# Optimization experiments

Measured on AMD Instinct MI355X. Metric: run time of the kernel, lower is better.

## Reference

```python
import jax, jax.numpy as jnp
import numpy as np

N = 50000   # total nodes
G = 100     # graphs
E = 64      # embedding size
L = 4       # message-passing layers
MU = 100000 # unary atoms
ME = 200000 # binary atoms (edges)


def setup_inputs() -> dict:
    key = jax.random.key(0)
    ks = jax.random.split(key, 16)

    def w(k, shape):
        fan_in = shape[0]
        return (jax.random.normal(k, shape, jnp.float32) / np.sqrt(fan_in)).astype(jnp.float32)

    inp = {
        "rel_unary": jax.random.randint(ks[0], (MU, 1), 0, N, dtype=jnp.int32),
        "rel_edge": jax.random.randint(ks[1], (ME, 2), 0, N, dtype=jnp.int32),
        "graph_ids": jnp.repeat(jnp.arange(G, dtype=jnp.int32), N // G),
        "num_graphs": G,
        # unary relation message MLP (E -> E -> E)
        "Wm1_u": w(ks[2], (E, E)), "bm1_u": jnp.zeros((E,), jnp.float32),
        "Wm2_u": w(ks[3], (E, E)), "bm2_u": jnp.zeros((E,), jnp.float32),
        # binary relation message MLP (2E -> 2E -> 2E), one message per argument position
        "Wm1_e": w(ks[4], (2 * E, 2 * E)), "bm1_e": jnp.zeros((2 * E,), jnp.float32),
        "Wm2_e": w(ks[5], (2 * E, 2 * E)), "bm2_e": jnp.zeros((2 * E,), jnp.float32),
        # node update MLP (2E -> E -> E)
        "Wu1": w(ks[6], (2 * E, E)), "bu1": jnp.zeros((E,), jnp.float32),
        "Wu2": w(ks[7], (E, E)), "bu2": jnp.zeros((E,), jnp.float32),
        # LayerNorm
        "ln_w": jnp.ones((E,), jnp.float32), "ln_b": jnp.zeros((E,), jnp.float32),
        # SumReadout projection (E -> E)
        "Wr": w(ks[8], (E, E)), "br": jnp.zeros((E,), jnp.float32),
        # global update MLP (2E -> E -> E)
        "Wg1": w(ks[9], (2 * E, E)), "bg1": jnp.zeros((E,), jnp.float32),
        "Wg2": w(ks[10], (E, E)), "bg2": jnp.zeros((E,), jnp.float32),
    }
    return inp


def _mlp(x, W1, b1, W2, b2):
    return jax.nn.relu(x @ W1 + b1) @ W2 + b2


def _ln(x, w, b):
    mu = x.mean(-1, keepdims=True)
    v = ((x - mu) ** 2).mean(-1, keepdims=True)
    return (x - mu) * jax.lax.rsqrt(v + 1e-5) * w + b


def reference(rel_unary, rel_edge, graph_ids, num_graphs,
              Wm1_u, bm1_u, Wm2_u, bm2_u,
              Wm1_e, bm1_e, Wm2_e, bm2_e,
              Wu1, bu1, Wu2, bu2,
              ln_w, ln_b, Wr, br,
              Wg1, bg1, Wg2, bg2):
    n = graph_ids.shape[0]
    e = ln_w.shape[0]
    me = rel_edge.shape[0]
    h = jnp.zeros((n, e), jnp.float32)  # initial node embeddings (as in torch code)
    for _ in range(L):
        # --- message: per-relation MLP over concatenated argument embeddings ---
        msg_u = _mlp(h[rel_unary[:, 0]], Wm1_u, bm1_u, Wm2_u, bm2_u)          # [MU, E]
        xe = h[rel_edge].reshape(me, 2 * e)                                    # [ME, 2E]
        msg_e = _mlp(xe, Wm1_e, bm1_e, Wm2_e, bm2_e).reshape(me * 2, e)        # one msg per arg
        # --- aggregation: scatter-sum messages to destination nodes ---
        all_msgs = jnp.concatenate([msg_u, msg_e], axis=0)
        all_idx = jnp.concatenate([rel_unary[:, 0], rel_edge.reshape(-1)], axis=0)
        agg = jax.ops.segment_sum(all_msgs, all_idx, num_segments=n)           # [N, E]
        # --- update MLP + LayerNorm ---
        nxt = _ln(_mlp(jnp.concatenate([h, agg], axis=1), Wu1, bu1, Wu2, bu2), ln_w, ln_b)
        # --- global readout + broadcast update ---
        g = jax.ops.segment_sum(h, graph_ids, num_segments=num_graphs) @ Wr + br  # [G, E]
        gin = jnp.concatenate([h, g[graph_ids]], axis=1)                       # repeat_interleave as gather
        gm = _ln(_mlp(gin, Wg1, bg1, Wg2, bg2), ln_w, ln_b)
        # residual update
        h = h + nxt + gm
    return h
```

## Files before the change

### kernel.cpp

```cpp
#include <hip/hip_runtime.h>


#define E 64
#define TWO_E 128

__device__ __forceinline__ void sfma32(float (&acc)[32], float xu, const float* w) {
  #pragma unroll
  for (int i = 0; i < 32; ++i) acc[i] = fmaf(xu, w[i], acc[i]);
}
__device__ __forceinline__ void sfma16(float (&acc)[16], float xu, const float* w) {
  #pragma unroll
  for (int i = 0; i < 16; ++i) acc[i] = fmaf(xu, w[i], acc[i]);
}

__global__ void k_zero(float4* __restrict__ p, int n4) {
  int i = blockIdx.x * blockDim.x + threadIdx.x;
  if (i < n4) p[i] = make_float4(0.f, 0.f, 0.f, 0.f);
}

__global__ void k_count_e(const int* __restrict__ rel_e, int* __restrict__ cpos0,
                          int* __restrict__ cpos1, int me) {
  int e = blockIdx.x * blockDim.x + threadIdx.x;
  if (e >= me) return;
  int2 sd = ((const int2*)rel_e)[e];
  atomicAdd(&cpos0[sd.x], 1);
  atomicAdd(&cpos1[sd.y], 1);
}
__global__ void k_count_u(const int* __restrict__ rel_u, int* __restrict__ cnt_u, int mu) {
  int m = blockIdx.x * blockDim.x + threadIdx.x;
  if (m >= mu) return;
  atomicAdd(&cnt_u[rel_u[m]], 1);
}

__global__ void __launch_bounds__(256) k_bsum(
    const int* __restrict__ cpos0, const int* __restrict__ cpos1,
    int* __restrict__ bsum, int nn, int nb) {
  __shared__ int l0[256], l1[256];
  int t = threadIdx.x, b = blockIdx.x;
  int i = b * 256 + t;
  l0[t] = (i < nn) ? cpos0[i] : 0;
  l1[t] = (i < nn) ? cpos1[i] : 0;
  __syncthreads();
  for (int off = 128; off > 0; off >>= 1) {
    if (t < off) { l0[t] += l0[t + off]; l1[t] += l1[t + off]; }
    __syncthreads();
  }
  if (t == 0) { bsum[b] = l0[0]; bsum[nb + b] = l1[0]; }
}

__global__ void __launch_bounds__(256) k_scanblk(
    const int* __restrict__ bsum, int* __restrict__ boff, int nb) {
  __shared__ int l0[256], l1[256];
  int t = threadIdx.x;
  int o0 = (t < nb) ? bsum[t] : 0;
  int o1 = (t < nb) ? bsum[nb + t] : 0;
  l0[t] = o0; l1[t] = o1;
  __syncthreads();
  for (int off = 1; off < 256; off <<= 1) {
    int v0 = (t >= off) ? l0[t - off] : 0;
    int v1 = (t >= off) ? l1[t - off] : 0;
    __syncthreads();
    l0[t] += v0; l1[t] += v1;
    __syncthreads();
  }
  if (t < nb) { boff[t] = l0[t] - o0; boff[nb + t] = l1[t] - o1; }
}

__global__ void __launch_bounds__(256) k_wstart(
    const int* __restrict__ cpos0, const int* __restrict__ cpos1,
    const int* __restrict__ boff,
    int* __restrict__ startp, int* __restrict__ startp0, int* __restrict__ startp1,
    int* __restrict__ cur0, int* __restrict__ cur1, int nn, int nb, int me) {
  __shared__ int l0[256], l1[256];
  int t = threadIdx.x, b = blockIdx.x;
  int i = b * 256 + t;
  int c0 = (i < nn) ? cpos0[i] : 0;
  int c1 = (i < nn) ? cpos1[i] : 0;
  l0[t] = c0; l1[t] = c1;
  __syncthreads();
  for (int off = 1; off < 256; off <<= 1) {
    int v0 = (t >= off) ? l0[t - off] : 0;
    int v1 = (t >= off) ? l1[t - off] : 0;
    __syncthreads();
    l0[t] += v0; l1[t] += v1;
    __syncthreads();
  }
  if (i < nn) {
    int s0 = boff[b] + l0[t] - c0;
    int s1 = boff[nb + b] + l1[t] - c1;
    startp0[i] = s0; startp1[i] = s1; startp[i] = s0 + s1;
    cur0[i] = s0; cur1[i] = s1;
  }
  if (i == nn) { startp0[nn] = me; startp1[nn] = me; startp[nn] = 2 * me; }
}

__global__ void k_fill_e(const int* __restrict__ rel_e,
                         const int* __restrict__ startp, const int* __restrict__ startp0,
                         const int* __restrict__ startp1, const int* __restrict__ cpos0,
                         int* __restrict__ cur0, int* __restrict__ cur1,
                         int* __restrict__ ord0, int* __restrict__ pos0,
                         int* __restrict__ posE1, int me) {
  int e = blockIdx.x * blockDim.x + threadIdx.x;
  if (e >= me) return;
  int2 sd = ((const int2*)rel_e)[e];
  int s = sd.x, d = sd.y;
  int i0 = atomicAdd(&cur0[s], 1);
  ord0[i0] = e;
  pos0[i0] = startp[s] + (i0 - startp0[s]);
  int i1 = atomicAdd(&cur1[d], 1);
  posE1[e] = startp[d] + cpos0[d] + (i1 - startp1[d]);
}

__global__ void k_mlp0(const float* __restrict__ b1u, const float* __restrict__ W2u,
                       const float* __restrict__ b2u,
                       const float* __restrict__ b1e, const float* __restrict__ W2e,
                       const float* __restrict__ b2e,
                       const float* __restrict__ br,
                       float* __restrict__ mu0, float* __restrict__ me0,
                       float* __restrict__ g, int gn) {
  __shared__ float hu[64], he[128];
  int t = threadIdx.x;
  if (t < 64) hu[t] = fmaxf(b1u[t], 0.f);
  he[t] = fmaxf(b1e[t], 0.f);
  __syncthreads();
  if (t < 64) {
    float a = b2u[t];
    for (int k = 0; k < 64; ++k) a = fmaf(hu[k], W2u[k * 64 + t], a);
    mu0[t] = a;
  }
  float a = b2e[t];
  for (int k = 0; k < 128; ++k) a = fmaf(he[k], W2e[k * TWO_E + t], a);
  me0[t] = a;
  if (t < 64) {
    float b = br[t];
    for (int gi = 0; gi < gn; ++gi) g[gi * 64 + t] = b;
  }
}

__global__ void k_agg0(const int* __restrict__ cnt_u, const int* __restrict__ cpos0,
                       const int* __restrict__ cpos1, const float* __restrict__ mu0,
                       const float* __restrict__ me0, float* __restrict__ agg, int nn) {
  int i = blockIdx.x * blockDim.x + threadIdx.x;
  int n = i >> 4, j4 = i & 15;
  if (n >= nn) return;
  float cu = (float)cnt_u[n], c0 = (float)cpos0[n], c1 = (float)cpos1[n];
  float4 m = ((const float4*)mu0)[j4];
  float4 a = ((const float4*)me0)[j4];
  float4 b = ((const float4*)(me0 + 64))[j4];
  ((float4*)agg)[i] = make_float4(cu * m.x + c0 * a.x + c1 * b.x,
                                  cu * m.y + c0 * a.y + c1 * b.y,
                                  cu * m.z + c0 * a.z + c1 * b.z,
                                  cu * m.w + c0 * a.w + c1 * b.w);
}

__global__ void __launch_bounds__(512) k_edge_pab(
    const int* __restrict__ rel_e, const int* __restrict__ ord0,
    const int* __restrict__ pos0, const int* __restrict__ posE1,
    const float* __restrict__ Pab,
    const float* __restrict__ W2, const float* __restrict__ b2,
    float* __restrict__ msgbuf, int me)
{
  __shared__ __align__(16) float tl[64 * 132];
  const int tid = threadIdx.x;
  const int lane = tid & 63;
  const int wq = __builtin_amdgcn_readfirstlane(tid >> 6);
  const int i = blockIdx.x * 64 + lane;
  const bool valid = (i < me);
  const int ic = valid ? i : (me - 1);
  const int e = ord0[ic];
  const int2 sd = ((const int2*)rel_e)[e];
  const int s = sd.x, d = sd.y;
  const int p_s = pos0[ic];
  const int p_d = posE1[e];

  {
    const float4* pa = (const float4*)(Pab + (size_t)s * 256 + wq * 16);
    const float4* pb = (const float4*)(Pab + (size_t)d * 256 + 128 + wq * 16);
    float4* trow = (float4*)&tl[lane * 132 + wq * 16];
    #pragma unroll
    for (int u = 0; u < 4; ++u) {
      float4 va = pa[u], vb = pb[u];
      trow[u] = make_float4(fmaxf(va.x + vb.x, 0.f), fmaxf(va.y + vb.y, 0.f),
                            fmaxf(va.z + vb.z, 0.f), fmaxf(va.w + vb.w, 0.f));
    }
  }
  __syncthreads();

  float o[16];
  {
    const float* bp = b2 + wq * 16;
    #pragma unroll
    for (int u = 0; u < 16; ++u) o[u] = bp[u];
  }
  {
    const float4* tr = (const float4*)&tl[lane * 132];
    const float* w = W2 + wq * 16;
    #pragma unroll 4
    for (int kk = 0; kk < 32; ++kk) {
      float4 tv = tr[kk];
      sfma16(o, tv.x, w);
      sfma16(o, tv.y, w + TWO_E);
      sfma16(o, tv.z, w + 2 * TWO_E);
      sfma16(o, tv.w, w + 3 * TWO_E);
      w += 4 * TWO_E;
    }
  }
  if (valid) {
    int p0 = (wq >= 4) ? p_d : p_s;
    float4* mp = (float4*)(msgbuf + (size_t)p0 * E + (wq & 3) * 16);
    #pragma unroll
    for (int u = 0; u < 4; ++u)
      mp[u] = make_float4(o[4*u], o[4*u+1], o[4*u+2], o[4*u+3]);
  }
}

__global__ void __launch_bounds__(256) k_edge_fb(
    const int* __restrict__ rel_e, const int* __restrict__ ord0,
    const int* __restrict__ pos0, const int* __restrict__ posE1,
    const float* __restrict__ h,
    const float* __restrict__ W1, const float* __restrict__ b1,
    const float* __restrict__ W2, const float* __restrict__ b2,
    float* __restrict__ msgbuf, int me)
{
  __shared__ __align__(16) float tl[64 * 132];
  const int tid = threadIdx.x;
  const int lane = tid & 63;
  const int wq = __builtin_amdgcn_readfirstlane(tid >> 6);
  const int i = blockIdx.x * 64 + lane;
  const bool valid = (i < me);
  const int ic = valid ? i : (me - 1);
  const int e = ord0[ic];
  const int2 sd = ((const int2*)rel_e)[e];
  const int s = sd.x, d = sd.y;
  const int p_s = pos0[ic];
  const int p_d = posE1[e];
  const float4* xs4 = (const float4*)(h + (size_t)s * E);
  const float4* xd4 = (const float4*)(h + (size_t)d * E);

  float acc[32];
  {
    const float* bp = b1 + wq * 32;
    #pragma unroll
    for (int u = 0; u < 32; ++u) acc[u] = bp[u];
  }
  {
    const float* w = W1 + wq * 32;
    #pragma unroll 2
    for (int k4 = 0; k4 < 16; ++k4) {
      float4 xv = xs4[k4];
      sfma32(acc, xv.x, w);
      sfma32(acc, xv.y, w + TWO_E);
      sfma32(acc, xv.z, w + 2 * TWO_E);
      sfma32(acc, xv.w, w + 3 * TWO_E);
      w += 4 * TWO_E;
    }
    #pragma unroll 2
    for (int k4 = 0; k4 < 16; ++k4) {
      float4 xv = xd4[k4];
      sfma32(acc, xv.x, w);
      sfma32(acc, xv.y, w + TWO_E);
      sfma32(acc, xv.z, w + 2 * TWO_E);
      sfma32(acc, xv.w, w + 3 * TWO_E);
      w += 4 * TWO_E;
    }
  }
  {
    float4* trow = (float4*)&tl[lane * 132 + wq * 32];
    #pragma unroll
    for (int u = 0; u < 8; ++u)
      trow[u] = make_float4(fmaxf(acc[4*u], 0.f), fmaxf(acc[4*u+1], 0.f),
                            fmaxf(acc[4*u+2], 0.f), fmaxf(acc[4*u+3], 0.f));
  }
  __syncthreads();

  float o[32];
  {
    const float* bp = b2 + wq * 32;
    #pragma unroll
    for (int u = 0; u < 32; ++u) o[u] = bp[u];
  }
  {
    const float4* tr = (const float4*)&tl[lane * 132];
    const float* w = W2 + wq * 32;
    #pragma unroll 4
    for (int kk = 0; kk < 32; ++kk) {
      float4 tv = tr[kk];
      sfma32(o, tv.x, w);
      sfma32(o, tv.y, w + TWO_E);
      sfma32(o, tv.z, w + 2 * TWO_E);
      sfma32(o, tv.w, w + 3 * TWO_E);
      w += 4 * TWO_E;
    }
  }
  if (valid) {
    int p0 = (wq >> 1) ? p_d : p_s;
    float4* mp = (float4*)(msgbuf + (size_t)p0 * E + (wq & 1) * 32);
    #pragma unroll
    for (int u = 0; u < 8; ++u)
      mp[u] = make_float4(o[4*u], o[4*u+1], o[4*u+2], o[4*u+3]);
  }
}

__global__ void __launch_bounds__(256) k_gather(
    const float* __restrict__ msgbuf, const int* __restrict__ startp,
    float* __restrict__ agg, int nn)
{
  int wave = threadIdx.x >> 6;
  int j = threadIdx.x & 63;
  int n = blockIdx.x * 4 + wave;
  if (n >= nn) return;
  int s0 = startp[n], s1 = startp[n + 1];
  int cnt = s1 - s0;
  const float* p = msgbuf + (size_t)s0 * E + j;
  float v0 = 0.f, v1 = 0.f;
  int i = 0;
  for (; i + 1 < cnt; i += 2) { v0 += p[0]; v1 += p[E]; p += 2 * E; }
  if (i < cnt) v0 += p[0];
  agg[(size_t)n * E + j] += v0 + v1;
}

__global__ void __launch_bounds__(256) k_readout_g(
    const float* __restrict__ h, const int* __restrict__ gids,
    const float* __restrict__ Wr, const float* __restrict__ br,
    float* __restrict__ g, int nn, int npg)
{
  __shared__ float ls[4][64];
  __shared__ float grow[64];
  const int j = threadIdx.x & 63;
  const int w = threadIdx.x >> 6;
  const int base = blockIdx.x * npg;
  float acc = 0.f;
  for (int i = w; i < npg; i += 4) {
    int node = base + i;
    if (node < nn) acc += h[(size_t)node * 64 + j];
  }
  ls[w][j] = acc;
  __syncthreads();
  if (w == 0) grow[j] = ls[0][j] + ls[1][j] + ls[2][j] + ls[3][j];
  __syncthreads();
  float p = 0.f;
  #pragma unroll
  for (int kk = 0; kk < 16; ++kk) {
    int k = w * 16 + kk;
    p = fmaf(grow[k], Wr[k * 64 + j], p);
  }
  ls[w][j] = p;
  __syncthreads();
  if (w == 0) {
    int gout = gids[base];
    g[gout * 64 + j] = ls[0][j] + ls[1][j] + ls[2][j] + ls[3][j] + br[j];
  }
}

template <bool DO_NEXT>
__global__ void __launch_bounds__(256) k_update(
    float* __restrict__ h, float* __restrict__ agg,
    const float* __restrict__ gvec, const int* __restrict__ gids,
    const float* __restrict__ Wu1, const float* __restrict__ bu1,
    const float* __restrict__ Wu2, const float* __restrict__ bu2,
    const float* __restrict__ Wg1, const float* __restrict__ bg1,
    const float* __restrict__ Wg2, const float* __restrict__ bg2,
    const float* __restrict__ lnw, const float* __restrict__ lnb,
    const int* __restrict__ cnt_u,
    const float* __restrict__ Wmu1, const float* __restrict__ bmu1,
    const float* __restrict__ Wmu2, const float* __restrict__ bmu2,
    const float* __restrict__ W1e, const float* __restrict__ b1e,
    float* __restrict__ Pab, int do_pab, int nn)
{
  __shared__ __align__(16) float tl[64 * 68];
  __shared__ float st[64 * 9];
  const int tid = threadIdx.x;
  const int lane = tid & 63;
  const int q = __builtin_amdgcn_readfirstlane(tid >> 6);
  const int n = blockIdx.x * 64 + lane;
  const bool valid = (n < nn);
  const int ncl = valid ? n : (nn - 1);
  const int gid = gids[ncl];
  const float4* hx = (const float4*)(h + (size_t)ncl * E);
  const float4* ax = (const float4*)(agg + (size_t)ncl * E);
  const float4* gx = (const float4*)(gvec + (size_t)gid * E);

  float res[16];

  #pragma unroll
  for (int pass = 0; pass < 2; ++pass) {
    const float* W1 = (pass == 0) ? Wu1 : Wg1;
    const float* B1 = (pass == 0) ? bu1 : bg1;
    const float* W2 = (pass == 0) ? Wu2 : Wg2;
    const float* B2 = (pass == 0) ? bu2 : bg2;
    const float4* xb = (pass == 0) ? ax : gx;

    float acc[16];
    {
      const float* bp = B1 + q * 16;
      #pragma unroll
      for (int u = 0; u < 16; ++u) acc[u] = bp[u];
    }
    {
      const float* w = W1 + q * 16;
      #pragma unroll 2
      for (int k4 = 0; k4 < 16; ++k4) {
        float4 xv = hx[k4];
        sfma16(acc, xv.x, w);
        sfma16(acc, xv.y, w + E);
        sfma16(acc, xv.z, w + 2 * E);
        sfma16(acc, xv.w, w + 3 * E);
        w += 4 * E;
      }
      #pragma unroll 2
      for (int k4 = 0; k4 < 16; ++k4) {
        float4 xv = xb[k4];
        sfma16(acc, xv.x, w);
        sfma16(acc, xv.y, w + E);
        sfma16(acc, xv.z, w + 2 * E);
        sfma16(acc, xv.w, w + 3 * E);
        w += 4 * E;
      }
    }
    {
      float4* trow = (float4*)&tl[lane * 68 + q * 16];
      #pragma unroll
      for (int u = 0; u < 4; ++u)
        trow[u] = make_float4(fmaxf(acc[4*u], 0.f), fmaxf(acc[4*u+1], 0.f),
                              fmaxf(acc[4*u+2], 0.f), fmaxf(acc[4*u+3], 0.f));
    }
    __syncthreads();

    float o[16];
    {
      const float* bp = B2 + q * 16;
      #pragma unroll
      for (int u = 0; u < 16; ++u) o[u] = bp[u];
    }
    {
      const float4* tr = (const float4*)&tl[lane * 68];
      const float* w = W2 + q * 16;
      #pragma unroll 4
      for (int kk = 0; kk < 16; ++kk) {
        float4 tv = tr[kk];
        sfma16(o, tv.x, w);
        sfma16(o, tv.y, w + E);
        sfma16(o, tv.z, w + 2 * E);
        sfma16(o, tv.w, w + 3 * E);
        w += 4 * E;
      }
    }

    float s1 = 0.f;
    #pragma unroll
    for (int u = 0; u < 16; ++u) s1 += o[u];
    st[lane * 9 + q] = s1;
    __syncthreads();
    float mu = (st[lane * 9 + 0] + st[lane * 9 + 1] +
                st[lane * 9 + 2] + st[lane * 9 + 3]) * (1.f / E);
    float s2 = 0.f;
    #pragma unroll
    for (int u = 0; u < 16; ++u) { float dm = o[u] - mu; s2 += dm * dm; }
    st[lane * 9 + 4 + q] = s2;
    __syncthreads();
    float var = (st[lane * 9 + 4] + st[lane * 9 + 5] +
                 st[lane * 9 + 6] + st[lane * 9 + 7]) * (1.f / E);
    float rs = rsqrtf(var + 1e-5f);
    {
      const float* lw = lnw + q * 16;
      const float* lb = lnb + q * 16;
      #pragma unroll
      for (int u = 0; u < 16; ++u) {
        float v = (o[u] - mu) * rs * lw[u] + lb[u];
        if (pass == 0) res[u] = v; else res[u] += v;
      }
    }
  }

  float hnew[16];
  {
    const float4* hr = (const float4*)(h + (size_t)ncl * E + q * 16);
    #pragma unroll
    for (int u = 0; u < 4; ++u) {
      float4 hv = hr[u];
      hnew[4*u+0] = hv.x + res[4*u+0];
      hnew[4*u+1] = hv.y + res[4*u+1];
      hnew[4*u+2] = hv.z + res[4*u+2];
      hnew[4*u+3] = hv.w + res[4*u+3];
    }
  }
  if (valid) {
    float4* hw = (float4*)(h + (size_t)n * E + q * 16);
    #pragma unroll
    for (int u = 0; u < 4; ++u)
      hw[u] = make_float4(hnew[4*u], hnew[4*u+1], hnew[4*u+2], hnew[4*u+3]);
  }

  if (DO_NEXT) {
    {
      float4* trow = (float4*)&tl[lane * 68 + q * 16];
      #pragma unroll
      for (int u = 0; u < 4; ++u)
        trow[u] = make_float4(hnew[4*u], hnew[4*u+1], hnew[4*u+2], hnew[4*u+3]);
    }
    __syncthreads();

    float acc[16];
    {
      const float* bp = bmu1 + q * 16;
      #pragma unroll
      for (int u = 0; u < 16; ++u) acc[u] = bp[u];
    }
    {
      const float4* tr = (const float4*)&tl[lane * 68];
      const float* w = Wmu1 + q * 16;
      #pragma unroll 4
      for (int kk = 0; kk < 16; ++kk) {
        float4 tv = tr[kk];
        sfma16(acc, tv.x, w);
        sfma16(acc, tv.y, w + E);
        sfma16(acc, tv.z, w + 2 * E);
        sfma16(acc, tv.w, w + 3 * E);
        w += 4 * E;
      }
    }

    if (do_pab) {
      #pragma unroll 1
      for (int c = 0; c < 2; ++c) {
        const int col = q * 64 + c * 32;
        const int rbase = (col < 128) ? 0 : 64;
        const int cw = (col < 128) ? col : (col - 128);
        float pacc[32];
        if (col < 128) {
          const float* bp = b1e + cw;
          #pragma unroll
          for (int u = 0; u < 32; ++u) pacc[u] = bp[u];
        } else {
          #pragma unroll
          for (int u = 0; u < 32; ++u) pacc[u] = 0.f;
        }
        const float4* tr = (const float4*)&tl[lane * 68];
        const float* w = W1e + rbase * TWO_E + cw;
        #pragma unroll 4
        for (int kk = 0; kk < 16; ++kk) {
          float4 tv = tr[kk];
          sfma32(pacc, tv.x, w);
          sfma32(pacc, tv.y, w + TWO_E);
          sfma32(pacc, tv.z, w + 2 * TWO_E);
          sfma32(pacc, tv.w, w + 3 * TWO_E);
          w += 4 * TWO_E;
        }
        if (valid) {
          float4* op = (float4*)(Pab + (size_t)n * 256 + col);
          #pragma unroll
          for (int u = 0; u < 8; ++u)
            op[u] = make_float4(pacc[4*u], pacc[4*u+1], pacc[4*u+2], pacc[4*u+3]);
        }
      }
    }
    __syncthreads();
    {
      float4* trow = (float4*)&tl[lane * 68 + q * 16];
      #pragma unroll
      for (int u = 0; u < 4; ++u)
        trow[u] = make_float4(fmaxf(acc[4*u], 0.f), fmaxf(acc[4*u+1], 0.f),
                              fmaxf(acc[4*u+2], 0.f), fmaxf(acc[4*u+3], 0.f));
    }
    __syncthreads();

    float o[16];
    {
      const float* bp = bmu2 + q * 16;
      #pragma unroll
      for (int u = 0; u < 16; ++u) o[u] = bp[u];
    }
    {
      const float4* tr = (const float4*)&tl[lane * 68];
      const float* w = Wmu2 + q * 16;
      #pragma unroll 4
      for (int kk = 0; kk < 16; ++kk) {
        float4 tv = tr[kk];
        sfma16(o, tv.x, w);
        sfma16(o, tv.y, w + E);
        sfma16(o, tv.z, w + 2 * E);
        sfma16(o, tv.w, w + 3 * E);
        w += 4 * E;
      }
    }
    if (valid) {
      float cf = (float)cnt_u[n];
      float4* ap = (float4*)(agg + (size_t)n * E + q * 16);
      #pragma unroll
      for (int u = 0; u < 4; ++u)
        ap[u] = make_float4(o[4*u] * cf, o[4*u+1] * cf, o[4*u+2] * cf, o[4*u+3] * cf);
    }
  }
}

extern "C" void kernel_launch(void* const* d_in, const int* in_sizes, int n_in,
                              void* d_out, int out_size, void* d_ws, size_t ws_size,
                              hipStream_t stream) {
  (void)n_in; (void)out_size;
  const int*   rel_u = (const int*)d_in[0];
  const int*   rel_e = (const int*)d_in[1];
  const int*   gids  = (const int*)d_in[2];
  const float* Wm1_u = (const float*)d_in[4];
  const float* bm1_u = (const float*)d_in[5];
  const float* Wm2_u = (const float*)d_in[6];
  const float* bm2_u = (const float*)d_in[7];
  const float* Wm1_e = (const float*)d_in[8];
  const float* bm1_e = (const float*)d_in[9];
  const float* Wm2_e = (const float*)d_in[10];
  const float* bm2_e = (const float*)d_in[11];
  const float* Wu1   = (const float*)d_in[12];
  const float* bu1   = (const float*)d_in[13];
  const float* Wu2   = (const float*)d_in[14];
  const float* bu2   = (const float*)d_in[15];
  const float* lnw   = (const float*)d_in[16];
  const float* lnb   = (const float*)d_in[17];
  const float* Wr    = (const float*)d_in[18];
  const float* br    = (const float*)d_in[19];
  const float* Wg1   = (const float*)d_in[20];
  const float* bg1   = (const float*)d_in[21];
  const float* Wg2   = (const float*)d_in[22];
  const float* bg2   = (const float*)d_in[23];

  const int MU_ = in_sizes[0];
  const int ME_ = in_sizes[1] / 2;
  const int NN  = in_sizes[2];
  const int GN  = 100;
  const int NPG = NN / GN;
  const int M2  = 2 * ME_;
  const int NB  = (NN + 255) / 256;
  const int NBW = (NN + 256) / 256;
  const int NBU = (NN + 63) / 64;

  float* h       = (float*)d_out;
  float* agg     = (float*)d_ws;
  float* g       = agg + (size_t)NN * E;
  float* mu0     = g + (size_t)GN * E;
  float* me0     = mu0 + 64;
  float* msgbuf  = me0 + TWO_E;
  int*   cpos0   = (int*)(msgbuf + (size_t)M2 * E);
  int*   cpos1   = cpos0 + NN;
  int*   cnt_u   = cpos1 + NN;
  int*   startp  = cnt_u + NN;
  int*   startp0 = startp + NN + 1;
  int*   startp1 = startp0 + NN + 1;
  int*   cur0    = startp1 + NN + 1;
  int*   cur1    = cur0 + NN + 1;
  int*   ord0    = cur1 + NN + 1;
  int*   pos0    = ord0 + ME_;
  int*   posE1   = pos0 + ME_;
  int*   bsum    = posE1 + ME_;
  int*   boff    = bsum + 2 * NB;
  size_t int_end = (size_t)(boff + 2 * NB - (int*)d_ws);
  size_t pab_off = (int_end + 3) & ~(size_t)3;
  float* Pab     = (float*)d_ws + pab_off;
  size_t need_pab = (pab_off + (size_t)NN * 256) * 4;
  const bool pab_mode = (ws_size >= need_pab);

  {
    int n4 = NN * E / 4;
    k_zero<<<(n4 + 255) / 256, 256, 0, stream>>>((float4*)h, n4);
  }
  {
    int n4 = (3 * NN + 4) / 4;
    k_zero<<<(n4 + 255) / 256, 256, 0, stream>>>((float4*)cpos0, n4);
  }
  k_count_e<<<(ME_ + 255) / 256, 256, 0, stream>>>(rel_e, cpos0, cpos1, ME_);
  k_count_u<<<(MU_ + 255) / 256, 256, 0, stream>>>(rel_u, cnt_u, MU_);
  k_bsum<<<NB, 256, 0, stream>>>(cpos0, cpos1, bsum, NN, NB);
  k_scanblk<<<1, 256, 0, stream>>>(bsum, boff, NB);
  k_wstart<<<NBW, 256, 0, stream>>>(cpos0, cpos1, boff, startp, startp0, startp1,
                                    cur0, cur1, NN, NB, ME_);
  k_fill_e<<<(ME_ + 255) / 256, 256, 0, stream>>>(
      rel_e, startp, startp0, startp1, cpos0, cur0, cur1, ord0, pos0, posE1, ME_);
  k_mlp0<<<1, 128, 0, stream>>>(bm1_u, Wm2_u, bm2_u, bm1_e, Wm2_e, bm2_e,
                                br, mu0, me0, g, GN);

  k_agg0<<<(NN * 16 + 255) / 256, 256, 0, stream>>>(cnt_u, cpos0, cpos1, mu0, me0, agg, NN);
  k_update<true><<<NBU, 256, 0, stream>>>(
      h, agg, g, gids, Wu1, bu1, Wu2, bu2, Wg1, bg1, Wg2, bg2, lnw, lnb,
      cnt_u, Wm1_u, bm1_u, Wm2_u, bm2_u, Wm1_e, bm1_e, Pab, pab_mode ? 1 : 0, NN);

  for (int l = 1; l < 4; ++l) {
    if (pab_mode)
      k_edge_pab<<<(ME_ + 63) / 64, 512, 0, stream>>>(
          rel_e, ord0, pos0, posE1, Pab, Wm2_e, bm2_e, msgbuf, ME_);
    else
      k_edge_fb<<<(ME_ + 63) / 64, 256, 0, stream>>>(
          rel_e, ord0, pos0, posE1, h, Wm1_e, bm1_e, Wm2_e, bm2_e, msgbuf, ME_);
    k_gather<<<(NN + 3) / 4, 256, 0, stream>>>(msgbuf, startp, agg, NN);
    k_readout_g<<<GN, 256, 0, stream>>>(h, gids, Wr, br, g, NN, NPG);
    if (l < 3)
      k_update<true><<<NBU, 256, 0, stream>>>(
          h, agg, g, gids, Wu1, bu1, Wu2, bu2, Wg1, bg1, Wg2, bg2, lnw, lnb,
          cnt_u, Wm1_u, bm1_u, Wm2_u, bm2_u, Wm1_e, bm1_e, Pab, pab_mode ? 1 : 0, NN);
    else
      k_update<false><<<NBU, 256, 0, stream>>>(
          h, agg, g, gids, Wu1, bu1, Wu2, bu2, Wg1, bg1, Wg2, bg2, lnw, lnb,
          cnt_u, Wm1_u, bm1_u, Wm2_u, bm2_u, Wm1_e, bm1_e, Pab, 0, NN);
  }
}
```

Before: 838.1 us.

## Run update and global MLPs concurrently on separate wave pairs in k_update

Previously all four waves ran the update MLP and then the global MLP in two sequential passes, each wave owning 16 output columns. Now waves 0-1 compute the update MLP and waves 2-3 the global MLP at the same time, each wave owning 32 columns, with a second LDS tile holding the global result for the residual sum. This halves the barrier-separated phases for the two MLPs but doubles per-thread accumulator registers and LDS use, which may lower occupancy.

```diff
diff --git a/kernel.cpp b/kernel.cpp
--- a/kernel.cpp
+++ b/kernel.cpp
@@ -367,163 +367,166 @@
     const float* __restrict__ W1e, const float* __restrict__ b1e,
     float* __restrict__ Pab, int do_pab, int nn)
 {
-  __shared__ __align__(16) float tl[64 * 68];
+  __shared__ __align__(16) float tlu[64 * 68];
+  __shared__ __align__(16) float tlg[64 * 68];
   __shared__ float st[64 * 9];
   const int tid = threadIdx.x;
   const int lane = tid & 63;
-  const int q = __builtin_amdgcn_readfirstlane(tid >> 6);
+  const int w = __builtin_amdgcn_readfirstlane(tid >> 6);
+  const int hf = w & 1;
+  const int pbase = w & 2;
+  const bool isU = (w < 2);
   const int n = blockIdx.x * 64 + lane;
   const bool valid = (n < nn);
   const int ncl = valid ? n : (nn - 1);
   const int gid = gids[ncl];
   const float4* hx = (const float4*)(h + (size_t)ncl * E);
-  const float4* ax = (const float4*)(agg + (size_t)ncl * E);
-  const float4* gx = (const float4*)(gvec + (size_t)gid * E);
-
-  float res[16];
-
-  #pragma unroll
-  for (int pass = 0; pass < 2; ++pass) {
-    const float* W1 = (pass == 0) ? Wu1 : Wg1;
-    const float* B1 = (pass == 0) ? bu1 : bg1;
-    const float* W2 = (pass == 0) ? Wu2 : Wg2;
-    const float* B2 = (pass == 0) ? bu2 : bg2;
-    const float4* xb = (pass == 0) ? ax : gx;
-
-    float acc[16];
+  const float4* xb = isU ? (const float4*)(agg + (size_t)ncl * E)
+                         : (const float4*)(gvec + (size_t)gid * E);
+  const float* W1 = isU ? Wu1 : Wg1;
+  const float* B1 = isU ? bu1 : bg1;
+  const float* W2 = isU ? Wu2 : Wg2;
+  const float* B2 = isU ? bu2 : bg2;
+  float* tlmine = isU ? tlu : tlg;
+
+  float acc[32];
+  {
+    const float* bp = B1 + hf * 32;
+    #pragma unroll
+    for (int u = 0; u < 32; ++u) acc[u] = bp[u];
+  }
+  {
+    const float* wp = W1 + hf * 32;
+    #pragma unroll 2
+    for (int k4 = 0; k4 < 16; ++k4) {
+      float4 xv = hx[k4];
+      sfma32(acc, xv.x, wp);
+      sfma32(acc, xv.y, wp + E);
+      sfma32(acc, xv.z, wp + 2 * E);
+      sfma32(acc, xv.w, wp + 3 * E);
+      wp += 4 * E;
+    }
+    #pragma unroll 2
+    for (int k4 = 0; k4 < 16; ++k4) {
+      float4 xv = xb[k4];
+      sfma32(acc, xv.x, wp);
+      sfma32(acc, xv.y, wp + E);
+      sfma32(acc, xv.z, wp + 2 * E);
+      sfma32(acc, xv.w, wp + 3 * E);
+      wp += 4 * E;
+    }
+  }
+  {
+    float4* trow = (float4*)&tlmine[lane * 68 + hf * 32];
+    #pragma unroll
+    for (int u = 0; u < 8; ++u)
+      trow[u] = make_float4(fmaxf(acc[4*u], 0.f), fmaxf(acc[4*u+1], 0.f),
+                            fmaxf(acc[4*u+2], 0.f), fmaxf(acc[4*u+3], 0.f));
+  }
+  __syncthreads();
+
+  float o[32];
+  {
+    const float* bp = B2 + hf * 32;
+    #pragma unroll
+    for (int u = 0; u < 32; ++u) o[u] = bp[u];
+  }
+  {
+    const float4* tr = (const float4*)&tlmine[lane * 68];
+    const float* wp = W2 + hf * 32;
+    #pragma unroll 4
+    for (int kk = 0; kk < 16; ++kk) {
+      float4 tv = tr[kk];
+      sfma32(o, tv.x, wp);
+      sfma32(o, tv.y, wp + E);
+      sfma32(o, tv.z, wp + 2 * E);
+      sfma32(o, tv.w, wp + 3 * E);
+      wp += 4 * E;
+    }
+  }
+
+  {
+    float s1 = 0.f;
+    #pragma unroll
+    for (int u = 0; u < 32; ++u) s1 += o[u];
+    st[lane * 9 + w] = s1;
+    __syncthreads();
+    float mu = (st[lane * 9 + pbase] + st[lane * 9 + pbase + 1]) * (1.f / E);
+    float s2 = 0.f;
+    #pragma unroll
+    for (int u = 0; u < 32; ++u) { float dm = o[u] - mu; s2 += dm * dm; }
+    st[lane * 9 + 4 + w] = s2;
+    __syncthreads();
+    float var = (st[lane * 9 + 4 + pbase] + st[lane * 9 + 5 + pbase]) * (1.f / E);
+    float rs = rsqrtf(var + 1e-5f);
+    const float* lw = lnw + hf * 32;
+    const float* lb = lnb + hf * 32;
+    #pragma unroll
+    for (int u = 0; u < 32; ++u)
+      o[u] = (o[u] - mu) * rs * lw[u] + lb[u];
+  }
+
+  if (!isU) {
+    float4* gp = (float4*)&tlg[lane * 68 + hf * 32];
+    #pragma unroll
+    for (int u = 0; u < 8; ++u)
+      gp[u] = make_float4(o[4*u], o[4*u+1], o[4*u+2], o[4*u+3]);
+  }
+  __syncthreads();
+
+  float hnew[32];
+  if (isU) {
+    const float4* gp = (const float4*)&tlg[lane * 68 + hf * 32];
+    const float4* hr = (const float4*)(h + (size_t)ncl * E + hf * 32);
+    #pragma unroll
+    for (int u = 0; u < 8; ++u) {
+      float4 hv = hr[u], gv = gp[u];
+      hnew[4*u+0] = hv.x + o[4*u+0] + gv.x;
+      hnew[4*u+1] = hv.y + o[4*u+1] + gv.y;
+      hnew[4*u+2] = hv.z + o[4*u+2] + gv.z;
+      hnew[4*u+3] = hv.w + o[4*u+3] + gv.w;
+    }
+    if (valid) {
+      float4* hw = (float4*)(h + (size_t)n * E + hf * 32);
+      #pragma unroll
+      for (int u = 0; u < 8; ++u)
+        hw[u] = make_float4(hnew[4*u], hnew[4*u+1], hnew[4*u+2], hnew[4*u+3]);
+    }
+  }
+
+  if (DO_NEXT) {
+    if (isU) {
+      float4* trow = (float4*)&tlu[lane * 68 + hf * 32];
+      #pragma unroll
+      for (int u = 0; u < 8; ++u)
+        trow[u] = make_float4(hnew[4*u], hnew[4*u+1], hnew[4*u+2], hnew[4*u+3]);
+    }
+    __syncthreads();
+
+    float uacc[16];
     {
-      const float* bp = B1 + q * 16;
+      const float* bp = bmu1 + w * 16;
       #pragma unroll
-      for (int u = 0; u < 16; ++u) acc[u] = bp[u];
+      for (int u = 0; u < 16; ++u) uacc[u] = bp[u];
     }
     {
-      const float* w = W1 + q * 16;
-      #pragma unroll 2
-      for (int k4 = 0; k4 < 16; ++k4) {
-        float4 xv = hx[k4];
-        sfma16(acc, xv.x, w);
-        sfma16(acc, xv.y, w + E);
-        sfma16(acc, xv.z, w + 2 * E);
-        sfma16(acc, xv.w, w + 3 * E);
-        w += 4 * E;
-      }
-      #pragma unroll 2
-      for (int k4 = 0; k4 < 16; ++k4) {
-        float4 xv = xb[k4];
-        sfma16(acc, xv.x, w);
-        sfma16(acc, xv.y, w + E);
-        sfma16(acc, xv.z, w + 2 * E);
-        sfma16(acc, xv.w, w + 3 * E);
-        w += 4 * E;
-      }
-    }
-    {
-      float4* trow = (float4*)&tl[lane * 68 + q * 16];
-      #pragma unroll
-      for (int u = 0; u < 4; ++u)
-        trow[u] = make_float4(fmaxf(acc[4*u], 0.f), fmaxf(acc[4*u+1], 0.f),
-                              fmaxf(acc[4*u+2], 0.f), fmaxf(acc[4*u+3], 0.f));
-    }
-    __syncthreads();
-
-    float o[16];
-    {
-      const float* bp = B2 + q * 16;
-      #pragma unroll
-      for (int u = 0; u < 16; ++u) o[u] = bp[u];
-    }
-    {
-      const float4* tr = (const float4*)&tl[lane * 68];
-      const float* w = W2 + q * 16;
+      const float4* tr = (const float4*)&tlu[lane * 68];
+      const float* wp = Wmu1 + w * 16;
       #pragma unroll 4
       for (int kk = 0; kk < 16; ++kk) {
         float4 tv = tr[kk];
-        sfma16(o, tv.x, w);
-        sfma16(o, tv.y, w + E);
-        sfma16(o, tv.z, w + 2 * E);
-        sfma16(o, tv.w, w + 3 * E);
-        w += 4 * E;
-      }
-    }
-
-    float s1 = 0.f;
-    #pragma unroll
-    for (int u = 0; u < 16; ++u) s1 += o[u];
-    st[lane * 9 + q] = s1;
-    __syncthreads();
-    float mu = (st[lane * 9 + 0] + st[lane * 9 + 1] +
-                st[lane * 9 + 2] + st[lane * 9 + 3]) * (1.f / E);
-    float s2 = 0.f;
-    #pragma unroll
-    for (int u = 0; u < 16; ++u) { float dm = o[u] - mu; s2 += dm * dm; }
-    st[lane * 9 + 4 + q] = s2;
-    __syncthreads();
-    float var = (st[lane * 9 + 4] + st[lane * 9 + 5] +
-                 st[lane * 9 + 6] + st[lane * 9 + 7]) * (1.f / E);
-    float rs = rsqrtf(var + 1e-5f);
-    {
-      const float* lw = lnw + q * 16;
-      const float* lb = lnb + q * 16;
-      #pragma unroll
-      for (int u = 0; u < 16; ++u) {
-        float v = (o[u] - mu) * rs * lw[u] + lb[u];
-        if (pass == 0) res[u] = v; else res[u] += v;
-      }
-    }
-  }
-
-  float hnew[16];
-  {
-    const float4* hr = (const float4*)(h + (size_t)ncl * E + q * 16);
-    #pragma unroll
-    for (int u = 0; u < 4; ++u) {
-      float4 hv = hr[u];
-      hnew[4*u+0] = hv.x + res[4*u+0];
-      hnew[4*u+1] = hv.y + res[4*u+1];
-      hnew[4*u+2] = hv.z + res[4*u+2];
-      hnew[4*u+3] = hv.w + res[4*u+3];
-    }
-  }
-  if (valid) {
-    float4* hw = (float4*)(h + (size_t)n * E + q * 16);
-    #pragma unroll
-    for (int u = 0; u < 4; ++u)
-      hw[u] = make_float4(hnew[4*u], hnew[4*u+1], hnew[4*u+2], hnew[4*u+3]);
-  }
-
-  if (DO_NEXT) {
-    {
-      float4* trow = (float4*)&tl[lane * 68 + q * 16];
-      #pragma unroll
-      for (int u = 0; u < 4; ++u)
-        trow[u] = make_float4(hnew[4*u], hnew[4*u+1], hnew[4*u+2], hnew[4*u+3]);
-    }
-    __syncthreads();
-
-    float acc[16];
-    {
-      const float* bp = bmu1 + q * 16;
-      #pragma unroll
-      for (int u = 0; u < 16; ++u) acc[u] = bp[u];
-    }
-    {
-      const float4* tr = (const float4*)&tl[lane * 68];
-      const float* w = Wmu1 + q * 16;
-      #pragma unroll 4
-      for (int kk = 0; kk < 16; ++kk) {
-        float4 tv = tr[kk];
-        sfma16(acc, tv.x, w);
-        sfma16(acc, tv.y, w + E);
-        sfma16(acc, tv.z, w + 2 * E);
-        sfma16(acc, tv.w, w + 3 * E);
-        w += 4 * E;
+        sfma16(uacc, tv.x, wp);
+        sfma16(uacc, tv.y, wp + E);
+        sfma16(uacc, tv.z, wp + 2 * E);
+        sfma16(uacc, tv.w, wp + 3 * E);
+        wp += 4 * E;
       }
     }
 
     if (do_pab) {
       #pragma unroll 1
       for (int c = 0; c < 2; ++c) {
-        const int col = q * 64 + c * 32;
+        const int col = w * 64 + c * 32;
         const int rbase = (col < 128) ? 0 : 64;
         const int cw = (col < 128) ? col : (col - 128);
         float pacc[32];
@@ -535,16 +538,16 @@
           #pragma unroll
           for (int u = 0; u < 32; ++u) pacc[u] = 0.f;
         }
-        const float4* tr = (const float4*)&tl[lane * 68];
-        const float* w = W1e + rbase * TWO_E + cw;
+        const float4* tr = (const float4*)&tlu[lane * 68];
+        const float* wp = W1e + rbase * TWO_E + cw;
         #pragma unroll 4
         for (int kk = 0; kk < 16; ++kk) {
           float4 tv = tr[kk];
-          sfma32(pacc, tv.x, w);
-          sfma32(pacc, tv.y, w + TWO_E);
-          sfma32(pacc, tv.z, w + 2 * TWO_E);
-          sfma32(pacc, tv.w, w + 3 * TWO_E);
-          w += 4 * TWO_E;
+          sfma32(pacc, tv.x, wp);
+          sfma32(pacc, tv.y, wp + TWO_E);
+          sfma32(pacc, tv.z, wp + 2 * TWO_E);
+          sfma32(pacc, tv.w, wp + 3 * TWO_E);
+          wp += 4 * TWO_E;
         }
         if (valid) {
           float4* op = (float4*)(Pab + (size_t)n * 256 + col);
@@ -555,40 +558,41 @@
       }
     }
     __syncthreads();
+
     {
-      float4* trow = (float4*)&tl[lane * 68 + q * 16];
+      float4* trow = (float4*)&tlg[lane * 68 + w * 16];
       #pragma unroll
       for (int u = 0; u < 4; ++u)
-        trow[u] = make_float4(fmaxf(acc[4*u], 0.f), fmaxf(acc[4*u+1], 0.f),
-                              fmaxf(acc[4*u+2], 0.f), fmaxf(acc[4*u+3], 0.f));
-    }
-    __syncthreads();
-
-    float o[16];
+        trow[u] = make_float4(fmaxf(uacc[4*u], 0.f), fmaxf(uacc[4*u+1], 0.f),
+                              fmaxf(uacc[4*u+2], 0.f), fmaxf(uacc[4*u+3], 0.f));
+    }
+    __syncthreads();
+
+    float uo[16];
     {
-      const float* bp = bmu2 + q * 16;
+      const float* bp = bmu2 + w * 16;
       #pragma unroll
-      for (int u = 0; u < 16; ++u) o[u] = bp[u];
+      for (int u = 0; u < 16; ++u) uo[u] = bp[u];
     }
     {
-      const float4* tr = (const float4*)&tl[lane * 68];
-      const float* w = Wmu2 + q * 16;
+      const float4* tr = (const float4*)&tlg[lane * 68];
+      const float* wp = Wmu2 + w * 16;
       #pragma unroll 4
       for (int kk = 0; kk < 16; ++kk) {
         float4 tv = tr[kk];
-        sfma16(o, tv.x, w);
-        sfma16(o, tv.y, w + E);
-        sfma16(o, tv.z, w + 2 * E);
-        sfma16(o, tv.w, w + 3 * E);
-        w += 4 * E;
+        sfma16(uo, tv.x, wp);
+        sfma16(uo, tv.y, wp + E);
+        sfma16(uo, tv.z, wp + 2 * E);
+        sfma16(uo, tv.w, wp + 3 * E);
+        wp += 4 * E;
       }
     }
     if (valid) {
       float cf = (float)cnt_u[n];
-      float4* ap = (float4*)(agg + (size_t)n * E + q * 16);
+      float4* ap = (float4*)(agg + (size_t)n * E + w * 16);
       #pragma unroll
       for (int u = 0; u < 4; ++u)
-        ap[u] = make_float4(o[4*u] * cf, o[4*u+1] * cf, o[4*u+2] * cf, o[4*u+3] * cf);
+        ap[u] = make_float4(uo[4*u] * cf, uo[4*u+1] * cf, uo[4*u+2] * cf, uo[4*u+3] * cf);
     }
   }
 }
```

Measured after the change: 815.7 us. 2.7% less time.
